# Optimization experiments

Hardware: AMD Instinct MI355X
Metric: run time of the kernel (lower is better)

## Reference

```python
import jax, jax.numpy as jnp
import numpy as np

N, F_IN, F_OUT = 200000, 128, 64
H, DEG = 50000, 32            # num_hyperedges, nodes per hyperedge
E = H * DEG                   # total incidences


def setup_inputs() -> dict:
    key = jax.random.key(0)
    k1, k2, k3, k4 = jax.random.split(key, 4)
    x = jax.random.normal(k1, (N, F_IN), dtype=jnp.float32)
    W = jax.random.normal(k2, (F_OUT, F_IN), dtype=jnp.float32) / np.sqrt(F_IN)
    a = jax.random.normal(k3, (2 * F_OUT,), dtype=jnp.float32) / np.sqrt(2 * F_OUT)
    nodes = jax.random.randint(k4, (E,), 0, N, dtype=jnp.int32)
    edges = jnp.repeat(jnp.arange(H, dtype=jnp.int32), DEG)  # sorted edge ids, DEG nodes each
    hyperedge_index = jnp.stack([nodes, edges])  # (2, E)
    return {"x": x, "W": W, "a": a, "hyperedge_index": hyperedge_index}


def reference(x, W, a, hyperedge_index):
    # h = W x  (Linear without bias, weight stored as (out, in))
    h = x @ W.T                                   # (N, F_OUT)
    nodes = hyperedge_index[0]
    eid = hyperedge_index[1]                      # sorted, groups incidences per hyperedge

    # attention score for ordered pair (j,k): a[:F] . h_j + a[F:] . h_k
    s1 = h @ a[:F_OUT]                            # (N,) left-slot contribution per node
    s2 = h @ a[F_OUT:]                            # (N,) right-slot contribution per node
    s1e = s1[nodes]                               # (E,)
    s2e = s2[nodes]                               # (E,)

    counts = jax.ops.segment_sum(jnp.ones_like(eid), eid, num_segments=H)   # degree per edge
    starts = jnp.cumsum(counts) - counts
    rank = jnp.arange(E, dtype=eid.dtype) - starts[eid]                     # position within edge
    deg_e = counts[eid]
    # sum over pairs j<k of (s1_j + s2_k):
    #   node at rank r appears (deg-1-r) times in left slot, r times in right slot
    w1 = (deg_e - 1 - rank).astype(h.dtype)
    w2 = rank.astype(h.dtype)
    pair_sum = jax.ops.segment_sum(s1e * w1 + s2e * w2, eid, num_segments=H)
    npairs = (counts * (counts - 1)) // 2
    edge_attention = pair_sum / jnp.maximum(npairs, 1).astype(h.dtype)      # mean over pairs
    # all H edges have DEG>=2 nodes by construction, matching torch's non-empty filter
    return h, edge_attention
```

## Files before the change

### kernel.cpp

```cpp
#include <hip/hip_runtime.h>

#define F_IN  128
#define F_OUT 64
#define DEG   32

typedef __attribute__((ext_vector_type(8))) short  short8;
typedef __attribute__((ext_vector_type(4))) float  float4v;

__device__ __forceinline__ unsigned short f2bf(float f) {
    unsigned int u = __builtin_bit_cast(unsigned int, f);
    u += 0x7FFFu + ((u >> 16) & 1u);
    return (unsigned short)(u >> 16);
}

__device__ __forceinline__ short8 load_cvt8(const float* __restrict__ p) {
    const float4v* q = (const float4v*)p;
    float4v lo = q[0];
    float4v hi = q[1];
    short8 r;
    r[0] = (short)f2bf(lo[0]); r[1] = (short)f2bf(lo[1]);
    r[2] = (short)f2bf(lo[2]); r[3] = (short)f2bf(lo[3]);
    r[4] = (short)f2bf(hi[0]); r[5] = (short)f2bf(hi[1]);
    r[6] = (short)f2bf(hi[2]); r[7] = (short)f2bf(hi[3]);
    return r;
}

__global__ __launch_bounds__(128) void gemm_s12_kernel(
    const float* __restrict__ x, const float* __restrict__ W,
    const float* __restrict__ a, float* __restrict__ h_out,
    float2* __restrict__ s12, int N)
{
    const int lane = threadIdx.x & 63;
    const int wave = threadIdx.x >> 6;
    const int wave_id = blockIdx.x * 2 + wave;
    const int row_base = wave_id * 32;
    if (row_base >= N) return;

    const int m = lane & 15;
    const int q = lane >> 4;

    short8 bfrag[4][4];
#pragma unroll
    for (int t = 0; t < 4; ++t) {
        const int n = m + 16 * t;
#pragma unroll
        for (int ks = 0; ks < 4; ++ks)
            bfrag[t][ks] = load_cvt8(W + n * F_IN + ks * 32 + q * 8);
    }

    float a1v[4], a2v[4];
#pragma unroll
    for (int t = 0; t < 4; ++t) {
        a1v[t] = a[m + 16 * t];
        a2v[t] = a[F_OUT + m + 16 * t];
    }

#pragma unroll
    for (int s = 0; s < 2; ++s) {
        const int row0 = row_base + s * 16;
        float4v acc[4];
#pragma unroll
        for (int t = 0; t < 4; ++t) acc[t] = (float4v){0.f, 0.f, 0.f, 0.f};

#pragma unroll
        for (int ks = 0; ks < 4; ++ks) {
            short8 afrag = load_cvt8(x + (size_t)(row0 + m) * F_IN + ks * 32 + q * 8);
#pragma unroll
            for (int t = 0; t < 4; ++t)
                acc[t] = __builtin_amdgcn_mfma_f32_16x16x32_bf16(
                            afrag, bfrag[t][ks], acc[t], 0, 0, 0);
        }

        const int rrow = row0 + q * 4;
        float p1[4] = {0.f, 0.f, 0.f, 0.f};
        float p2[4] = {0.f, 0.f, 0.f, 0.f};
#pragma unroll
        for (int t = 0; t < 4; ++t) {
            const int col = m + 16 * t;
#pragma unroll
            for (int r = 0; r < 4; ++r) {
                const float v = acc[t][r];
                h_out[(size_t)(rrow + r) * F_OUT + col] = v;
                p1[r] += v * a1v[t];
                p2[r] += v * a2v[t];
            }
        }
#pragma unroll
        for (int d = 1; d < 16; d <<= 1) {
#pragma unroll
            for (int r = 0; r < 4; ++r) {
                p1[r] += __shfl_xor(p1[r], d);
                p2[r] += __shfl_xor(p2[r], d);
            }
        }
        if (m == 0) {
#pragma unroll
            for (int r = 0; r < 4; ++r)
                s12[rrow + r] = make_float2(p1[r], p2[r]);
        }
    }
}

__global__ __launch_bounds__(256) void edge_att_kernel(
    const int* __restrict__ nodes, const float2* __restrict__ s12,
    float* __restrict__ eatt, int H)
{
    const int t = blockIdx.x * 256 + threadIdx.x;
    const int e = t >> 5;
    const int r = t & 31;
    if (e >= H) return;
    const int node = nodes[(size_t)e * DEG + r];
    const float2 s = s12[node];
    float v = s.x * (float)(DEG - 1 - r) + s.y * (float)r;
#pragma unroll
    for (int d = 1; d < 32; d <<= 1) v += __shfl_xor(v, d);
    if (r == 0) eatt[e] = v * (1.0f / 496.0f);
}

extern "C" void kernel_launch(void* const* d_in, const int* in_sizes, int n_in,
                              void* d_out, int out_size, void* d_ws, size_t ws_size,
                              hipStream_t stream)
{
    const float* x   = (const float*)d_in[0];
    const float* W   = (const float*)d_in[1];
    const float* a   = (const float*)d_in[2];
    const int*   hei = (const int*)d_in[3];

    const int N = in_sizes[0] / F_IN;
    const int E = in_sizes[3] / 2;
    const int H = E / DEG;
    const int* nodes = hei;

    float*  h_out = (float*)d_out;
    float*  eatt  = (float*)d_out + (size_t)N * F_OUT;
    float2* s12   = (float2*)d_ws;

    const int waves  = (N + 31) / 32;
    const int blocks = (waves + 1) / 2;
    gemm_s12_kernel<<<blocks, 128, 0, stream>>>(x, W, a, h_out, s12, N);

    const int eblocks = (E + 255) / 256;
    edge_att_kernel<<<eblocks, 256, 0, stream>>>(nodes, s12, eatt, H);
}
```

Baseline: 209.1 us.

## Stage bf16 W fragments in shared memory and batch x row loads

Converts W to bf16 MFMA fragments once per 256-thread block into LDS, instead of each wave loading and converting all of W into registers. This frees about 64 VGPRs per thread for better occupancy. All four k-slices of x are now issued as loads up front before the MFMA chain, to raise memory-level parallelism. Block size grows to four waves. The trade-off is an LDS read per MFMA and a block-wide barrier at kernel start.

```diff
diff --git a/kernel.cpp b/kernel.cpp
--- a/kernel.cpp
+++ b/kernel.cpp
@@ -13,10 +13,7 @@
     return (unsigned short)(u >> 16);
 }
 
-__device__ __forceinline__ short8 load_cvt8(const float* __restrict__ p) {
-    const float4v* q = (const float4v*)p;
-    float4v lo = q[0];
-    float4v hi = q[1];
+__device__ __forceinline__ short8 cvt8(float4v lo, float4v hi) {
     short8 r;
     r[0] = (short)f2bf(lo[0]); r[1] = (short)f2bf(lo[1]);
     r[2] = (short)f2bf(lo[2]); r[3] = (short)f2bf(lo[3]);
@@ -25,28 +22,40 @@
     return r;
 }
 
-__global__ __launch_bounds__(128) void gemm_s12_kernel(
+__device__ __forceinline__ short8 load_cvt8(const float* __restrict__ p) {
+    const float4v* q = (const float4v*)p;
+    return cvt8(q[0], q[1]);
+}
+
+__global__ __launch_bounds__(256) void gemm_s12_kernel(
     const float* __restrict__ x, const float* __restrict__ W,
     const float* __restrict__ a, float* __restrict__ h_out,
     float2* __restrict__ s12, int N)
 {
-    const int lane = threadIdx.x & 63;
-    const int wave = threadIdx.x >> 6;
-    const int wave_id = blockIdx.x * 2 + wave;
-    const int row_base = wave_id * 32;
+    __shared__ short8 wfrag[1024];
+
+    const int tid = threadIdx.x;
+
+#pragma unroll
+    for (int i0 = 0; i0 < 1024; i0 += 256) {
+        const int i     = i0 + tid;
+        const int combo = i >> 6;
+        const int sl    = i & 63;
+        const int t  = combo >> 2;
+        const int ks = combo & 3;
+        const int n  = (sl & 15) + 16 * t;
+        const int qq = sl >> 4;
+        wfrag[i] = load_cvt8(W + n * F_IN + ks * 32 + qq * 8);
+    }
+    __syncthreads();
+
+    const int lane = tid & 63;
+    const int wave = tid >> 6;
+    const int row_base = (blockIdx.x * 4 + wave) * 32;
     if (row_base >= N) return;
 
     const int m = lane & 15;
     const int q = lane >> 4;
-
-    short8 bfrag[4][4];
-#pragma unroll
-    for (int t = 0; t < 4; ++t) {
-        const int n = m + 16 * t;
-#pragma unroll
-        for (int ks = 0; ks < 4; ++ks)
-            bfrag[t][ks] = load_cvt8(W + n * F_IN + ks * 32 + q * 8);
-    }
 
     float a1v[4], a2v[4];
 #pragma unroll
@@ -58,17 +67,30 @@
 #pragma unroll
     for (int s = 0; s < 2; ++s) {
         const int row0 = row_base + s * 16;
+        const float* rowp = x + (size_t)(row0 + m) * F_IN + q * 8;
+
+        float4v raw[4][2];
+#pragma unroll
+        for (int ks = 0; ks < 4; ++ks) {
+            const float4v* p = (const float4v*)(rowp + ks * 32);
+            raw[ks][0] = p[0];
+            raw[ks][1] = p[1];
+        }
+        short8 afrag[4];
+#pragma unroll
+        for (int ks = 0; ks < 4; ++ks) afrag[ks] = cvt8(raw[ks][0], raw[ks][1]);
+
         float4v acc[4];
 #pragma unroll
         for (int t = 0; t < 4; ++t) acc[t] = (float4v){0.f, 0.f, 0.f, 0.f};
 
 #pragma unroll
         for (int ks = 0; ks < 4; ++ks) {
-            short8 afrag = load_cvt8(x + (size_t)(row0 + m) * F_IN + ks * 32 + q * 8);
 #pragma unroll
-            for (int t = 0; t < 4; ++t)
+            for (int t = 0; t < 4; ++t) {
                 acc[t] = __builtin_amdgcn_mfma_f32_16x16x32_bf16(
-                            afrag, bfrag[t][ks], acc[t], 0, 0, 0);
+                            afrag[ks], wfrag[(t * 4 + ks) * 64 + lane], acc[t], 0, 0, 0);
+            }
         }
 
         const int rrow = row0 + q * 4;
@@ -136,8 +158,8 @@
     float2* s12   = (float2*)d_ws;
 
     const int waves  = (N + 31) / 32;
-    const int blocks = (waves + 1) / 2;
-    gemm_s12_kernel<<<blocks, 128, 0, stream>>>(x, W, a, h_out, s12, N);
+    const int blocks = (waves + 3) / 4;
+    gemm_s12_kernel<<<blocks, 256, 0, stream>>>(x, W, a, h_out, s12, N);
 
     const int eblocks = (E + 255) / 256;
     edge_att_kernel<<<eblocks, 256, 0, stream>>>(nodes, s12, eatt, H);
```

New measurement: 190.6 us. -8.9%, faster.
